# Performance work log

Hardware: AMD Instinct MI355X
Metric: run time of the kernel (lower is better)

The kernel has to match this reference:

```python
import jax, jax.numpy as jnp
import numpy as np

N = 32768          # total nodes
B = 64             # number of graphs (batch.max()+1)
IN_C = 256
OUT_C = 256
NUM_SCALES = 4
NUM_HEADS = 8
BN_EPS = 1e-5


def setup_inputs() -> dict:
    key = jax.random.key(0)
    ks = jax.random.split(key, 10)
    out_s = OUT_C // NUM_SCALES
    x = jax.random.normal(ks[0], (N, IN_C), jnp.float32)
    spectral = jax.random.normal(ks[1], (NUM_SCALES, N, IN_C), jnp.float32)
    batch = jnp.sort(jax.random.randint(ks[2], (N,), 0, B)).astype(jnp.int64)
    # per-scale Linear weights (glorot) and zero biases; stored as [S, in, out_s]
    g = (6.0 / (IN_C + out_s)) ** 0.5
    Ws = jax.random.uniform(ks[3], (NUM_SCALES, IN_C, out_s), jnp.float32, -g, g)
    bs = jnp.zeros((NUM_SCALES, out_s), jnp.float32)
    # MultiheadAttention params (torch layout: in_proj [3E,E], out_proj [E,E])
    s_in = (1.0 / OUT_C) ** 0.5
    W_in = jax.random.uniform(ks[4], (3 * OUT_C, OUT_C), jnp.float32, -s_in, s_in)
    b_in = jnp.zeros((3 * OUT_C,), jnp.float32)
    W_out = jax.random.uniform(ks[5], (OUT_C, OUT_C), jnp.float32, -s_in, s_in)
    b_out = jnp.zeros((OUT_C,), jnp.float32)
    gamma = jnp.ones((OUT_C,), jnp.float32)
    beta = jnp.zeros((OUT_C,), jnp.float32)
    return {"x": x, "spectral": spectral, "Ws": Ws, "bs": bs,
            "W_in": W_in, "b_in": b_in, "W_out": W_out, "b_out": b_out,
            "gamma": gamma, "beta": beta, "batch": batch}


def _forward(x, spectral, Ws, bs, W_in, b_in, W_out, b_out, gamma, beta, batch):
    n, E = x.shape[0], W_out.shape[0]
    # per-scale linear on (x + spectral_feat), concat over scales -> [N, E]
    scale_out = jnp.einsum('sni,sio->sno', x[None] + spectral, Ws) + bs[:, None, :]
    h = jnp.moveaxis(scale_out, 0, 1).reshape(n, E)
    # ragged -> dense padding (batch is sorted segment ids)
    counts = jnp.bincount(batch, length=B)
    max_nodes = int(np.asarray(counts).max())  # data-dependent pad, as in torch
    starts = jnp.concatenate([jnp.zeros((1,), counts.dtype), jnp.cumsum(counts)[:-1]])
    pos = jnp.arange(n) - starts[batch]
    h_pad = jnp.zeros((B, max_nodes, E), h.dtype).at[batch, pos].set(h)
    # MHA over padded graphs (no key-padding mask, matching the source)
    hd = E // NUM_HEADS
    qkv = h_pad @ W_in.T + b_in                       # [B, M, 3E]
    q, k, v = jnp.split(qkv, 3, axis=-1)
    def heads(t):
        return t.reshape(B, max_nodes, NUM_HEADS, hd).transpose(0, 2, 1, 3)
    q, k, v = heads(q) * (hd ** -0.5), heads(k), heads(v)
    attn = jax.nn.softmax(jnp.einsum('bhqd,bhkd->bhqk', q, k), axis=-1)
    ctx = jnp.einsum('bhqk,bhkd->bhqd', attn, v)
    ctx = ctx.transpose(0, 2, 1, 3).reshape(B, max_nodes, E)
    h_att = ctx @ W_out.T + b_out
    # dense -> ragged unpad
    h2 = h_att[batch, pos]                            # [N, E]
    # BatchNorm1d (training-mode batch stats, deterministic) + ReLU; dropout=eval
    mean = h2.mean(axis=0)
    var = h2.var(axis=0)
    hn = (h2 - mean) * jax.lax.rsqrt(var + BN_EPS) * gamma + beta
    return jax.nn.relu(hn)


def reference(x, spectral, Ws, bs, W_in, b_in, W_out, b_out, gamma, beta, batch):
    return _forward(x, spectral, Ws, bs, W_in, b_in, W_out, b_out, gamma, beta, batch)
```

## Files before the change

### kernel.cpp

```cpp
#include <hip/hip_runtime.h>


typedef __attribute__((ext_vector_type(8))) short frag8;
typedef __attribute__((ext_vector_type(4))) float f32x4;
typedef __attribute__((ext_vector_type(8))) unsigned short ushort8;

#define NN 32768
#define NB 64
#define CIN 256
#define COUT 256
#define NHEAD 8
#define HD 32

#define BM 128
#define BN 64
#define BK 64
#define LDK 72
#define KT 128

__device__ inline unsigned short f2bf(float f) {
  unsigned u = __builtin_bit_cast(unsigned, f);
  u += 0x7FFFu + ((u >> 16) & 1u);
  return (unsigned short)(u >> 16);
}
__device__ inline float bf2f(unsigned short h) {
  return __builtin_bit_cast(float, (unsigned)h << 16);
}

__global__ void k_bounds(const int* __restrict__ batch, int* __restrict__ meta) {
  int i = blockIdx.x * 256 + threadIdx.x;
  if (i >= NN) return;
  int v = batch[i];
  int prev = (i == 0) ? -1 : batch[i - 1];
  for (int bb = prev + 1; bb <= v; ++bb) meta[NB + bb] = i;
}
__global__ void k_meta2(int* __restrict__ meta) {
  __shared__ int mx[NB];
  int b = threadIdx.x;
  int s = meta[NB + b];
  int e = (b == 63) ? NN : meta[NB + b + 1];
  meta[b] = e - s;
  mx[b] = e - s;
  __syncthreads();
  if (b == 0) {
    int m = 0;
    for (int j = 0; j < NB; ++j) m = max(m, mx[j]);
    meta[2 * NB] = m;
  }
}

__global__ void k_prep(const float* __restrict__ Ws, const float* __restrict__ Win,
                       const float* __restrict__ Wout,
                       unsigned short* __restrict__ wst, unsigned short* __restrict__ winb,
                       unsigned short* __restrict__ woutb) {
  int tid = blockIdx.x * 256 + threadIdx.x;
  if (tid < 4 * 64 * 256) {
    int s = tid >> 14, rem = tid & 16383, o = rem >> 8, i = rem & 255;
    wst[tid] = f2bf(Ws[((s * 256) + i) * 64 + o]);
  } else if (tid < 4 * 64 * 256 + 768 * 256) {
    int t2 = tid - 4 * 64 * 256;
    winb[t2] = f2bf(Win[t2]);
  } else if (tid < 4 * 64 * 256 + 768 * 256 + 256 * 256) {
    int t3 = tid - (4 * 64 * 256 + 768 * 256);
    woutb[t3] = f2bf(Wout[t3]);
  }
}

__device__ inline void mfma_tile(const unsigned short (*As)[LDK],
                                 const unsigned short (*Bs)[LDK],
                                 f32x4 acc[2][4], int wave, int lane) {
  int m16 = lane & 15, quad = lane >> 4;
#pragma unroll
  for (int kk = 0; kk < 2; ++kk) {
    frag8 a[2], b[4];
#pragma unroll
    for (int mi = 0; mi < 2; ++mi)
      a[mi] = *(const frag8*)&As[wave * 32 + mi * 16 + m16][kk * 32 + quad * 8];
#pragma unroll
    for (int ni = 0; ni < 4; ++ni)
      b[ni] = *(const frag8*)&Bs[ni * 16 + m16][kk * 32 + quad * 8];
#pragma unroll
    for (int mi = 0; mi < 2; ++mi)
#pragma unroll
      for (int ni = 0; ni < 4; ++ni)
        acc[mi][ni] = __builtin_amdgcn_mfma_f32_16x16x32_bf16(a[mi], b[ni], acc[mi][ni], 0, 0, 0);
  }
}

__device__ inline void stage_B64(const unsigned short* __restrict__ Wt, int c0, int k0,
                                 unsigned short (*Bs)[LDK], int t) {
  int n = t & 63, seg = t >> 6;
  const unsigned short* src = Wt + (size_t)(c0 + n) * 256 + k0 + seg * 16;
  uint4 v0 = *(const uint4*)src;
  uint4 v1 = *(const uint4*)(src + 8);
  *(uint4*)&Bs[n][seg * 16] = v0;
  *(uint4*)&Bs[n][seg * 16 + 8] = v1;
}

__device__ inline void stage_A_bf(const unsigned short* __restrict__ A, int lda, int r0, int k0,
                                  unsigned short (*As)[LDK], int t) {
  int r = t >> 1, half = t & 1;
  const unsigned short* src = A + (size_t)(r0 + r) * lda + k0 + half * 32;
#pragma unroll
  for (int i = 0; i < 4; ++i) {
    uint4 v = *(const uint4*)(src + i * 8);
    *(uint4*)&As[r][half * 32 + i * 8] = v;
  }
}

__global__ __launch_bounds__(256) void k_scale(const float* __restrict__ x,
                                               const float* __restrict__ spec,
                                               const unsigned short* __restrict__ wst,
                                               const float* __restrict__ bs,
                                               unsigned short* __restrict__ h) {
  __shared__ unsigned short As[BM][LDK];
  __shared__ unsigned short Bs[BN][LDK];
  int t = threadIdx.x, lane = t & 63, wave = t >> 6;
  int r0 = blockIdx.x * BM, s = blockIdx.y;
  f32x4 z = {0.f, 0.f, 0.f, 0.f};
  f32x4 acc[2][4];
#pragma unroll
  for (int mi = 0; mi < 2; ++mi)
#pragma unroll
    for (int ni = 0; ni < 4; ++ni) acc[mi][ni] = z;

  const float* sb = spec + (size_t)s * NN * CIN;
  for (int k0 = 0; k0 < CIN; k0 += BK) {
    {
      int r = t >> 1, half = t & 1;
      const float* xs = x + (size_t)(r0 + r) * CIN + k0 + half * 32;
      const float* ss = sb + (size_t)(r0 + r) * CIN + k0 + half * 32;
#pragma unroll
      for (int i = 0; i < 8; ++i) {
        float4 xv = *(const float4*)(xs + i * 4);
        float4 sv = *(const float4*)(ss + i * 4);
        ushort4 o;
        o.x = f2bf(xv.x + sv.x); o.y = f2bf(xv.y + sv.y);
        o.z = f2bf(xv.z + sv.z); o.w = f2bf(xv.w + sv.w);
        *(ushort4*)&As[r][half * 32 + i * 4] = o;
      }
    }
    stage_B64(wst + (size_t)s * 64 * 256, 0, k0, Bs, t);
    __syncthreads();
    mfma_tile(As, Bs, acc, wave, lane);
    __syncthreads();
  }
  int m16 = lane & 15, quad = lane >> 4;
#pragma unroll
  for (int mi = 0; mi < 2; ++mi)
#pragma unroll
    for (int ni = 0; ni < 4; ++ni) {
      int col = ni * 16 + m16;
      float bias = bs[s * 64 + col];
#pragma unroll
      for (int r = 0; r < 4; ++r) {
        int row = r0 + wave * 32 + mi * 16 + quad * 4 + r;
        h[(size_t)row * COUT + s * 64 + col] = f2bf(acc[mi][ni][r] + bias);
      }
    }
}

template <int LDOUT, bool F32OUT, bool STATS>
__global__ __launch_bounds__(256) void k_lin(const unsigned short* __restrict__ A,
                                             const unsigned short* __restrict__ Wt,
                                             const float* __restrict__ bias,
                                             void* __restrict__ out,
                                             float* __restrict__ sums) {
  __shared__ unsigned short As[BM][LDK];
  __shared__ unsigned short Bs[BN][LDK];
  int t = threadIdx.x, lane = t & 63, wave = t >> 6;
  int r0 = blockIdx.x * BM, c0 = blockIdx.y * BN;
  f32x4 z = {0.f, 0.f, 0.f, 0.f};
  f32x4 acc[2][4];
#pragma unroll
  for (int mi = 0; mi < 2; ++mi)
#pragma unroll
    for (int ni = 0; ni < 4; ++ni) acc[mi][ni] = z;

  for (int k0 = 0; k0 < 256; k0 += BK) {
    stage_A_bf(A, 256, r0, k0, As, t);
    stage_B64(Wt, c0, k0, Bs, t);
    __syncthreads();
    mfma_tile(As, Bs, acc, wave, lane);
    __syncthreads();
  }
  int m16 = lane & 15, quad = lane >> 4;
  float cs[4], cs2[4];
#pragma unroll
  for (int ni = 0; ni < 4; ++ni) { cs[ni] = 0.f; cs2[ni] = 0.f; }
#pragma unroll
  for (int mi = 0; mi < 2; ++mi)
#pragma unroll
    for (int ni = 0; ni < 4; ++ni) {
      int col = c0 + ni * 16 + m16;
      float bv = bias[col];
#pragma unroll
      for (int r = 0; r < 4; ++r) {
        int row = r0 + wave * 32 + mi * 16 + quad * 4 + r;
        float v = acc[mi][ni][r] + bv;
        if constexpr (STATS) { cs[ni] += v; cs2[ni] += v * v; }
        if constexpr (F32OUT)
          ((float*)out)[(size_t)row * LDOUT + col] = v;
        else
          ((unsigned short*)out)[(size_t)row * LDOUT + col] = f2bf(v);
      }
    }
  if constexpr (STATS) {
#pragma unroll
    for (int ni = 0; ni < 4; ++ni) {
      float a = cs[ni], b2 = cs2[ni];
      a += __shfl_xor(a, 16); a += __shfl_xor(a, 32);
      b2 += __shfl_xor(b2, 16); b2 += __shfl_xor(b2, 32);
      if (quad == 0) {
        atomicAdd(&sums[c0 + ni * 16 + m16], a);
        atomicAdd(&sums[256 + c0 + ni * 16 + m16], b2);
      }
    }
  }
}

__global__ __launch_bounds__(256) void k_attn_mfma(const unsigned short* __restrict__ qkv,
                                                   const int* __restrict__ meta,
                                                   unsigned short* __restrict__ ctx) {
  int b = blockIdx.x >> 3, head = blockIdx.x & 7;
  int c = meta[b], st = meta[NB + b], M = meta[2 * NB];
  int q0 = blockIdx.y * 128;
  if (q0 >= c) return;

  __shared__ unsigned short Vt[32][KT + 8];
  __shared__ unsigned short Pl[4][32][KT + 8];

  int t = threadIdx.x, lane = t & 63, wave = t >> 6;
  int m16 = lane & 15, quad = lane >> 4;
  const float SCALE = 0.17677669529663687f;
  float extra = (float)(M - c);

  int qbase = q0 + wave * 32;
  frag8 qf[2];
#pragma unroll
  for (int qg = 0; qg < 2; ++qg) {
    int qrow = qbase + qg * 16 + m16;
    qf[qg] = *(const frag8*)(qkv + (size_t)(st + qrow) * 768 + head * 32 + quad * 8);
  }

  f32x4 zz = {0.f, 0.f, 0.f, 0.f};
  f32x4 O[2][2];
  float lp[2][4];
#pragma unroll
  for (int qg = 0; qg < 2; ++qg) {
    O[qg][0] = zz; O[qg][1] = zz;
#pragma unroll
    for (int r = 0; r < 4; ++r) lp[qg][r] = 0.f;
  }

  for (int kt = 0; kt < c; kt += KT) {
    {
      int key = t >> 1, dh0 = (t & 1) * 16;
      const unsigned short* vp = qkv + (size_t)(st + kt + key) * 768 + 512 + head * 32 + dh0;
      ushort8 v0 = *(const ushort8*)vp;
      ushort8 v1 = *(const ushort8*)(vp + 8);
#pragma unroll
      for (int i = 0; i < 8; ++i) {
        Vt[dh0 + i][key] = v0[i];
        Vt[dh0 + 8 + i][key] = v1[i];
      }
    }
    __syncthreads();

#pragma unroll
    for (int sub = 0; sub < 4; ++sub) {
      int ks = kt + sub * 32;
      frag8 kf[2];
#pragma unroll
      for (int hf = 0; hf < 2; ++hf) {
        int krow = ks + hf * 16 + m16;
        kf[hf] = *(const frag8*)(qkv + (size_t)(st + krow) * 768 + 256 + head * 32 + quad * 8);
      }
#pragma unroll
      for (int qg = 0; qg < 2; ++qg)
#pragma unroll
        for (int hf = 0; hf < 2; ++hf) {
          f32x4 s = __builtin_amdgcn_mfma_f32_16x16x32_bf16(qf[qg], kf[hf], zz, 0, 0, 0);
          int key = ks + hf * 16 + m16;
          float msk = (key < c) ? 1.f : 0.f;
#pragma unroll
          for (int r = 0; r < 4; ++r) {
            float p = msk * __expf(s[r] * SCALE);
            lp[qg][r] += p;
            Pl[wave][qg * 16 + quad * 4 + r][sub * 32 + hf * 16 + m16] = f2bf(p);
          }
        }
    }
    __syncthreads();

#pragma unroll
    for (int sub = 0; sub < 4; ++sub) {
      frag8 vf[2];
#pragma unroll
      for (int dh = 0; dh < 2; ++dh)
        vf[dh] = *(const frag8*)&Vt[dh * 16 + m16][sub * 32 + quad * 8];
#pragma unroll
      for (int qg = 0; qg < 2; ++qg) {
        frag8 pf = *(const frag8*)&Pl[wave][qg * 16 + m16][sub * 32 + quad * 8];
#pragma unroll
        for (int dh = 0; dh < 2; ++dh)
          O[qg][dh] = __builtin_amdgcn_mfma_f32_16x16x32_bf16(pf, vf[dh], O[qg][dh], 0, 0, 0);
      }
    }
    __syncthreads();
  }

#pragma unroll
  for (int qg = 0; qg < 2; ++qg)
#pragma unroll
    for (int r = 0; r < 4; ++r) {
      float v = lp[qg][r];
      v += __shfl_xor(v, 1, 16);
      v += __shfl_xor(v, 2, 16);
      v += __shfl_xor(v, 4, 16);
      v += __shfl_xor(v, 8, 16);
      lp[qg][r] = v;
    }

#pragma unroll
  for (int qg = 0; qg < 2; ++qg)
#pragma unroll
    for (int r = 0; r < 4; ++r) {
      int qrow = qbase + qg * 16 + quad * 4 + r;
      if (qrow < c) {
        float inv = 1.f / (lp[qg][r] + extra);
        unsigned short* op = ctx + (size_t)(st + qrow) * 256 + head * 32;
        op[m16] = f2bf(O[qg][0][r] * inv);
        op[16 + m16] = f2bf(O[qg][1][r] * inv);
      }
    }
}

__global__ void k_bn_final(const float* __restrict__ sums, const float* __restrict__ gamma,
                           const float* __restrict__ beta, float* __restrict__ bnp) {
  int c = threadIdx.x;
  float mean = sums[c] * (1.0f / NN);
  float var = sums[256 + c] * (1.0f / NN) - mean * mean;
  float sc = rsqrtf(var + 1e-5f) * gamma[c];
  bnp[c] = sc;
  bnp[256 + c] = beta[c] - mean * sc;
}

__global__ __launch_bounds__(256) void k_bn_apply(const float* __restrict__ h,
                                                  const float* __restrict__ bnp,
                                                  float* __restrict__ out) {
  size_t i4 = (size_t)blockIdx.x * 256 + threadIdx.x;
  float4 v = *(const float4*)(h + i4 * 4);
  int c = (int)((i4 * 4) & 255);
  float4 sc = *(const float4*)(bnp + c);
  float4 sh = *(const float4*)(bnp + 256 + c);
  float4 r;
  r.x = fmaxf(v.x * sc.x + sh.x, 0.f);
  r.y = fmaxf(v.y * sc.y + sh.y, 0.f);
  r.z = fmaxf(v.z * sc.z + sh.z, 0.f);
  r.w = fmaxf(v.w * sc.w + sh.w, 0.f);
  *(float4*)(out + i4 * 4) = r;
}

extern "C" void kernel_launch(void* const* d_in, const int* in_sizes, int n_in,
                              void* d_out, int out_size, void* d_ws, size_t ws_size,
                              hipStream_t stream) {
  const float* x      = (const float*)d_in[0];
  const float* spec   = (const float*)d_in[1];
  const float* Ws     = (const float*)d_in[2];
  const float* bs     = (const float*)d_in[3];
  const float* Win    = (const float*)d_in[4];
  const float* b_in   = (const float*)d_in[5];
  const float* Wout   = (const float*)d_in[6];
  const float* b_out  = (const float*)d_in[7];
  const float* gamma  = (const float*)d_in[8];
  const float* beta   = (const float*)d_in[9];
  const int* batch    = (const int*)d_in[10];
  float* out = (float*)d_out;

  char* w = (char*)d_ws;
  size_t off = 0;
  auto alloc = [&](size_t bytes) -> void* {
    off = (off + 255) & ~(size_t)255;
    void* p = w + off; off += bytes; return p;
  };
  int* meta             = (int*)alloc(129 * sizeof(int));
  unsigned short* wst   = (unsigned short*)alloc((size_t)4 * 64 * 256 * 2);
  unsigned short* winb  = (unsigned short*)alloc((size_t)768 * 256 * 2);
  unsigned short* woutb = (unsigned short*)alloc((size_t)256 * 256 * 2);
  float* sums           = (float*)alloc(512 * 4);
  float* bnp            = (float*)alloc(512 * 4);
  unsigned short* h     = (unsigned short*)alloc((size_t)NN * 256 * 2);
  unsigned short* qkv   = (unsigned short*)alloc((size_t)NN * 768 * 2);
  unsigned short* ctx   = (unsigned short*)alloc((size_t)NN * 256 * 2);
  float* hatt           = (float*)alloc((size_t)NN * 256 * 4);

  hipMemsetAsync(sums, 0, 512 * 4, stream);
  k_bounds<<<NN / 256, 256, 0, stream>>>(batch, meta);
  k_meta2<<<1, 64, 0, stream>>>(meta);
  k_prep<<<1280, 256, 0, stream>>>(Ws, Win, Wout, wst, winb, woutb);
  k_scale<<<dim3(NN / BM, 4), 256, 0, stream>>>(x, spec, wst, bs, h);
  k_lin<768, false, false><<<dim3(NN / BM, 12), 256, 0, stream>>>(h, winb, b_in, qkv, nullptr);
  k_attn_mfma<<<dim3(NB * NHEAD, 8), 256, 0, stream>>>(qkv, meta, ctx);
  k_lin<256, true, true><<<dim3(NN / BM, 4), 256, 0, stream>>>(ctx, woutb, b_out, hatt, sums);
  k_bn_final<<<1, 256, 0, stream>>>(sums, gamma, beta, bnp);
  k_bn_apply<<<NN * 256 / 1024, 256, 0, stream>>>(hatt, bnp, out);
}
```

Before: 454.9 us.

## Widen linear GEMM tiles and keep attention probabilities in registers

```diff
diff --git a/kernel.cpp b/kernel.cpp
--- a/kernel.cpp
+++ b/kernel.cpp
@@ -13,7 +13,6 @@
 #define HD 32
 
 #define BM 128
-#define BN 64
 #define BK 64
 #define LDK 72
 #define KT 128
@@ -23,8 +22,8 @@
   u += 0x7FFFu + ((u >> 16) & 1u);
   return (unsigned short)(u >> 16);
 }
-__device__ inline float bf2f(unsigned short h) {
-  return __builtin_bit_cast(float, (unsigned)h << 16);
+__device__ inline unsigned pack2bf(float a, float b) {
+  return (unsigned)f2bf(a) | ((unsigned)f2bf(b) << 16);
 }
 
 __global__ void k_bounds(const int* __restrict__ batch, int* __restrict__ meta) {
@@ -66,23 +65,24 @@
   }
 }
 
+template <int NT>
 __device__ inline void mfma_tile(const unsigned short (*As)[LDK],
                                  const unsigned short (*Bs)[LDK],
-                                 f32x4 acc[2][4], int wave, int lane) {
+                                 f32x4 acc[2][NT], int wave, int lane) {
   int m16 = lane & 15, quad = lane >> 4;
 #pragma unroll
   for (int kk = 0; kk < 2; ++kk) {
-    frag8 a[2], b[4];
+    frag8 a[2], b[NT];
 #pragma unroll
     for (int mi = 0; mi < 2; ++mi)
       a[mi] = *(const frag8*)&As[wave * 32 + mi * 16 + m16][kk * 32 + quad * 8];
 #pragma unroll
-    for (int ni = 0; ni < 4; ++ni)
+    for (int ni = 0; ni < NT; ++ni)
       b[ni] = *(const frag8*)&Bs[ni * 16 + m16][kk * 32 + quad * 8];
 #pragma unroll
     for (int mi = 0; mi < 2; ++mi)
 #pragma unroll
-      for (int ni = 0; ni < 4; ++ni)
+      for (int ni = 0; ni < NT; ++ni)
         acc[mi][ni] = __builtin_amdgcn_mfma_f32_16x16x32_bf16(a[mi], b[ni], acc[mi][ni], 0, 0, 0);
   }
 }
@@ -97,6 +97,17 @@
   *(uint4*)&Bs[n][seg * 16 + 8] = v1;
 }
 
+__device__ inline void stage_B128(const unsigned short* __restrict__ Wt, int c0, int k0,
+                                  unsigned short (*Bs)[LDK], int t) {
+  int n = t >> 1, half = t & 1;
+  const unsigned short* src = Wt + (size_t)(c0 + n) * 256 + k0 + half * 32;
+#pragma unroll
+  for (int i = 0; i < 4; ++i) {
+    uint4 v = *(const uint4*)(src + i * 8);
+    *(uint4*)&Bs[n][half * 32 + i * 8] = v;
+  }
+}
+
 __device__ inline void stage_A_bf(const unsigned short* __restrict__ A, int lda, int r0, int k0,
                                   unsigned short (*As)[LDK], int t) {
   int r = t >> 1, half = t & 1;
@@ -114,7 +125,7 @@
                                                const float* __restrict__ bs,
                                                unsigned short* __restrict__ h) {
   __shared__ unsigned short As[BM][LDK];
-  __shared__ unsigned short Bs[BN][LDK];
+  __shared__ unsigned short Bs[64][LDK];
   int t = threadIdx.x, lane = t & 63, wave = t >> 6;
   int r0 = blockIdx.x * BM, s = blockIdx.y;
   f32x4 z = {0.f, 0.f, 0.f, 0.f};
@@ -142,7 +153,7 @@
     }
     stage_B64(wst + (size_t)s * 64 * 256, 0, k0, Bs, t);
     __syncthreads();
-    mfma_tile(As, Bs, acc, wave, lane);
+    mfma_tile<4>(As, Bs, acc, wave, lane);
     __syncthreads();
   }
   int m16 = lane & 15, quad = lane >> 4;
@@ -167,31 +178,31 @@
                                              void* __restrict__ out,
                                              float* __restrict__ sums) {
   __shared__ unsigned short As[BM][LDK];
-  __shared__ unsigned short Bs[BN][LDK];
+  __shared__ unsigned short Bs[128][LDK];
   int t = threadIdx.x, lane = t & 63, wave = t >> 6;
-  int r0 = blockIdx.x * BM, c0 = blockIdx.y * BN;
+  int r0 = blockIdx.x * BM, c0 = blockIdx.y * 128;
   f32x4 z = {0.f, 0.f, 0.f, 0.f};
-  f32x4 acc[2][4];
+  f32x4 acc[2][8];
 #pragma unroll
   for (int mi = 0; mi < 2; ++mi)
 #pragma unroll
-    for (int ni = 0; ni < 4; ++ni) acc[mi][ni] = z;
+    for (int ni = 0; ni < 8; ++ni) acc[mi][ni] = z;
 
   for (int k0 = 0; k0 < 256; k0 += BK) {
     stage_A_bf(A, 256, r0, k0, As, t);
-    stage_B64(Wt, c0, k0, Bs, t);
-    __syncthreads();
-    mfma_tile(As, Bs, acc, wave, lane);
+    stage_B128(Wt, c0, k0, Bs, t);
+    __syncthreads();
+    mfma_tile<8>(As, Bs, acc, wave, lane);
     __syncthreads();
   }
   int m16 = lane & 15, quad = lane >> 4;
-  float cs[4], cs2[4];
-#pragma unroll
-  for (int ni = 0; ni < 4; ++ni) { cs[ni] = 0.f; cs2[ni] = 0.f; }
+  float cs[8], cs2[8];
+#pragma unroll
+  for (int ni = 0; ni < 8; ++ni) { cs[ni] = 0.f; cs2[ni] = 0.f; }
 #pragma unroll
   for (int mi = 0; mi < 2; ++mi)
 #pragma unroll
-    for (int ni = 0; ni < 4; ++ni) {
+    for (int ni = 0; ni < 8; ++ni) {
       int col = c0 + ni * 16 + m16;
       float bv = bias[col];
 #pragma unroll
@@ -207,7 +218,7 @@
     }
   if constexpr (STATS) {
 #pragma unroll
-    for (int ni = 0; ni < 4; ++ni) {
+    for (int ni = 0; ni < 8; ++ni) {
       float a = cs[ni], b2 = cs2[ni];
       a += __shfl_xor(a, 16); a += __shfl_xor(a, 32);
       b2 += __shfl_xor(b2, 16); b2 += __shfl_xor(b2, 32);
@@ -228,7 +239,6 @@
   if (q0 >= c) return;
 
   __shared__ unsigned short Vt[32][KT + 8];
-  __shared__ unsigned short Pl[4][32][KT + 8];
 
   int t = threadIdx.x, lane = t & 63, wave = t >> 6;
   int m16 = lane & 15, quad = lane >> 4;
@@ -245,13 +255,12 @@
 
   f32x4 zz = {0.f, 0.f, 0.f, 0.f};
   f32x4 O[2][2];
-  float lp[2][4];
-#pragma unroll
-  for (int qg = 0; qg < 2; ++qg) {
-    O[qg][0] = zz; O[qg][1] = zz;
-#pragma unroll
-    for (int r = 0; r < 4; ++r) lp[qg][r] = 0.f;
-  }
+  float lp[2] = {0.f, 0.f};
+#pragma unroll
+  for (int qg = 0; qg < 2; ++qg) { O[qg][0] = zz; O[qg][1] = zz; }
+
+  int sl0 = m16 + ((quad & 1) << 5);
+  int sl1 = sl0 + 16;
 
   for (int kt = 0; kt < c; kt += KT) {
     {
@@ -272,36 +281,43 @@
       int ks = kt + sub * 32;
       frag8 kf[2];
 #pragma unroll
-      for (int hf = 0; hf < 2; ++hf) {
-        int krow = ks + hf * 16 + m16;
-        kf[hf] = *(const frag8*)(qkv + (size_t)(st + krow) * 768 + 256 + head * 32 + quad * 8);
-      }
+      for (int kh = 0; kh < 2; ++kh) {
+        int krow = ks + kh * 16 + m16;
+        kf[kh] = *(const frag8*)(qkv + (size_t)(st + krow) * 768 + 256 + head * 32 + quad * 8);
+      }
+      unsigned pk[2][2][2];
 #pragma unroll
       for (int qg = 0; qg < 2; ++qg)
 #pragma unroll
-        for (int hf = 0; hf < 2; ++hf) {
-          f32x4 s = __builtin_amdgcn_mfma_f32_16x16x32_bf16(qf[qg], kf[hf], zz, 0, 0, 0);
-          int key = ks + hf * 16 + m16;
-          float msk = (key < c) ? 1.f : 0.f;
+        for (int kh = 0; kh < 2; ++kh) {
+          f32x4 s = __builtin_amdgcn_mfma_f32_16x16x32_bf16(kf[kh], qf[qg], zz, 0, 0, 0);
+          float p[4];
 #pragma unroll
           for (int r = 0; r < 4; ++r) {
-            float p = msk * __expf(s[r] * SCALE);
-            lp[qg][r] += p;
-            Pl[wave][qg * 16 + quad * 4 + r][sub * 32 + hf * 16 + m16] = f2bf(p);
+            int key = ks + kh * 16 + quad * 4 + r;
+            float msk = (key < c) ? 1.f : 0.f;
+            p[r] = msk * __expf(s[r] * SCALE);
+            lp[qg] += p[r];
           }
+          pk[qg][kh][0] = pack2bf(p[0], p[1]);
+          pk[qg][kh][1] = pack2bf(p[2], p[3]);
         }
-    }
-    __syncthreads();
-
-#pragma unroll
-    for (int sub = 0; sub < 4; ++sub) {
       frag8 vf[2];
 #pragma unroll
       for (int dh = 0; dh < 2; ++dh)
         vf[dh] = *(const frag8*)&Vt[dh * 16 + m16][sub * 32 + quad * 8];
 #pragma unroll
       for (int qg = 0; qg < 2; ++qg) {
-        frag8 pf = *(const frag8*)&Pl[wave][qg * 16 + m16][sub * 32 + quad * 8];
+        unsigned a0 = __shfl(pk[qg][0][0], sl0), a1 = __shfl(pk[qg][0][1], sl0);
+        unsigned a2 = __shfl(pk[qg][0][0], sl1), a3 = __shfl(pk[qg][0][1], sl1);
+        unsigned b0 = __shfl(pk[qg][1][0], sl0), b1 = __shfl(pk[qg][1][1], sl0);
+        unsigned b2 = __shfl(pk[qg][1][0], sl1), b3 = __shfl(pk[qg][1][1], sl1);
+        uint4 pw;
+        pw.x = (quad < 2) ? a0 : b0;
+        pw.y = (quad < 2) ? a1 : b1;
+        pw.z = (quad < 2) ? a2 : b2;
+        pw.w = (quad < 2) ? a3 : b3;
+        frag8 pf = __builtin_bit_cast(frag8, pw);
 #pragma unroll
         for (int dh = 0; dh < 2; ++dh)
           O[qg][dh] = __builtin_amdgcn_mfma_f32_16x16x32_bf16(pf, vf[dh], O[qg][dh], 0, 0, 0);
@@ -311,24 +327,21 @@
   }
 
 #pragma unroll
-  for (int qg = 0; qg < 2; ++qg)
-#pragma unroll
-    for (int r = 0; r < 4; ++r) {
-      float v = lp[qg][r];
-      v += __shfl_xor(v, 1, 16);
-      v += __shfl_xor(v, 2, 16);
-      v += __shfl_xor(v, 4, 16);
-      v += __shfl_xor(v, 8, 16);
-      lp[qg][r] = v;
-    }
+  for (int qg = 0; qg < 2; ++qg) {
+    float v = lp[qg];
+    v += __shfl_xor(v, 16);
+    v += __shfl_xor(v, 32);
+    lp[qg] = v;
+  }
 
 #pragma unroll
   for (int qg = 0; qg < 2; ++qg)
 #pragma unroll
     for (int r = 0; r < 4; ++r) {
       int qrow = qbase + qg * 16 + quad * 4 + r;
+      float lsum = __shfl(lp[qg], quad * 4 + r);
       if (qrow < c) {
-        float inv = 1.f / (lp[qg][r] + extra);
+        float inv = 1.f / (lsum + extra);
         unsigned short* op = ctx + (size_t)(st + qrow) * 256 + head * 32;
         op[m16] = f2bf(O[qg][0][r] * inv);
         op[16 + m16] = f2bf(O[qg][1][r] * inv);
@@ -400,9 +413,9 @@
   k_meta2<<<1, 64, 0, stream>>>(meta);
   k_prep<<<1280, 256, 0, stream>>>(Ws, Win, Wout, wst, winb, woutb);
   k_scale<<<dim3(NN / BM, 4), 256, 0, stream>>>(x, spec, wst, bs, h);
-  k_lin<768, false, false><<<dim3(NN / BM, 12), 256, 0, stream>>>(h, winb, b_in, qkv, nullptr);
+  k_lin<768, false, false><<<dim3(NN / BM, 6), 256, 0, stream>>>(h, winb, b_in, qkv, nullptr);
   k_attn_mfma<<<dim3(NB * NHEAD, 8), 256, 0, stream>>>(qkv, meta, ctx);
-  k_lin<256, true, true><<<dim3(NN / BM, 4), 256, 0, stream>>>(ctx, woutb, b_out, hatt, sums);
+  k_lin<256, true, true><<<dim3(NN / BM, 2), 256, 0, stream>>>(ctx, woutb, b_out, hatt, sums);
   k_bn_final<<<1, 256, 0, stream>>>(sums, gamma, beta, bnp);
   k_bn_apply<<<NN * 256 / 1024, 256, 0, stream>>>(hatt, bnp, out);
 }
```

After: 440.7 us. 3.1% less time.
